# Optimization experiments

Measured on AMD Instinct MI355X. Metric: run time of the kernel, lower is better.

The kernel has to match this reference:

```python
import jax, jax.numpy as jnp
import numpy as np

IN_CH = 64
NODE = 48
K_NEIGS = 10
KERNEL = 5
STRIDE = 2
BN_EPS = 1e-5


def _local_kernel(size, k, s):
    idx = np.arange(size * size).reshape(size, size)
    win = np.lib.stride_tricks.sliding_window_view(idx, (k, k))[::s, ::s]
    patches = win.reshape(-1, k * k)  # [n_edges, k*k] pixel indices
    n_edges = patches.shape[0]
    H = np.zeros((size * size, n_edges), dtype=np.float32)
    H[patches.reshape(-1), np.repeat(np.arange(n_edges), k * k)] = 1.0
    return jnp.asarray(H)


def _pairwise_distance(x):
    # (B,N,C) -> (B,N,N) squared euclidean
    xsq = jnp.sum(x * x, axis=-1, keepdims=True)
    return xsq - 2.0 * jnp.einsum('bnc,bmc->bnm', x, x) + jnp.swapaxes(xsq, 1, 2)


def _batched_knn(x, k):
    d = _pairwise_distance(x)
    avg = d.mean(-1, keepdims=True)
    neg_vals, inds = jax.lax.top_k(-d, k + 1)  # smallest k+1, sorted ascending
    return -neg_vals, inds, d, avg


def _incidence(inds, N):
    # weights_function(prob=False) == ones; scatter ones then transpose
    B, _, K = inds.shape
    b = jnp.arange(B)[:, None, None]
    p = jnp.arange(N)[None, :, None]
    M = jnp.zeros((B, N, N), dtype=jnp.float32).at[b, p, inds].set(1.0)
    return jnp.swapaxes(M, 1, 2)


def _generate_G(H):
    # G = diag(DV^-0.5) @ H @ I @ diag(DE^-1) @ H^T @ diag(DV^-0.5)
    DV = H.sum(axis=2)  # (B,N)
    DE = H.sum(axis=1)  # (B,E)
    dv2 = DV ** -0.5
    Hs = H * (1.0 / DE)[:, None, :]
    M = jnp.einsum('bne,bme->bnm', Hs, H)
    return dv2[:, :, None] * M * dv2[:, None, :]


def _build_G(x, local_H):
    B, N, C = x.shape
    _, topk_inds, _, _ = _batched_knn(x, K_NEIGS)
    H1 = _incidence(topk_inds, N)
    Dv = H1.sum(axis=2, keepdims=True)  # alpha = 1.0
    max_k = int(jnp.max(Dv))  # data-dependent width (eager, matches torch)
    _, ti2, _, _ = _batched_knn(x, max_k - 1)  # (B,N,max_k)
    tk = jnp.arange(max_k)[None, None, :]
    rng = jnp.broadcast_to(jnp.arange(N)[None, :, None], (B, N, max_k))
    new_inds = jnp.where(tk >= Dv, rng, ti2)
    new_H = _incidence(new_inds, N)
    loc = jnp.broadcast_to(local_H[None], (B,) + local_H.shape)
    return _generate_G(jnp.concatenate([new_H, loc], axis=2))


def _hgnn(x, G, W, b, gamma, beta):
    h = jnp.einsum('bnc,oc->bno', x, W) + b  # Linear
    h = jnp.einsum('bnm,bmc->bnc', G, h)
    mean = h.mean(axis=(0, 1))  # BatchNorm1d over (B,N) per channel
    var = h.var(axis=(0, 1))
    h = gamma * (h - mean) / jnp.sqrt(var + BN_EPS) + beta
    return jax.nn.relu(h) + x


def setup_inputs() -> dict:
    key = jax.random.key(0)
    k1, k2, k3 = jax.random.split(key, 3)
    B, N, C = 4, NODE * NODE, IN_CH
    x = jax.random.normal(k1, (B, N, C), dtype=jnp.float32)
    W = jax.random.normal(k2, (C, C), dtype=jnp.float32) / np.sqrt(C)
    b = jax.random.normal(k3, (C,), dtype=jnp.float32) * 0.01
    gamma = jnp.ones((C,), dtype=jnp.float32)
    beta = jnp.zeros((C,), dtype=jnp.float32)
    return {"x": x, "W": W, "b": b, "gamma": gamma, "beta": beta}


def reference(x, W, b, gamma, beta):
    local_H = _local_kernel(NODE, KERNEL, STRIDE)
    G = _build_G(x, local_H)  # graph construction is no_grad in torch
    return _hgnn(x, G, W, b, gamma, beta)
```

## Files before the change

### kernel.cpp

```cpp
#include <hip/hip_runtime.h>


#define HB    4
#define HN    2304
#define HC    64
#define HK    11
#define HL    48
#define HW    22
#define HE2   484
#define HE    (HN + HE2)
#define HRPB  4
#define NSLOT 36
#define NPAIRS (HB * HK * HN)

__global__ void hg14_sentinel(float* out, int n) {
    int i = blockIdx.x * 256 + threadIdx.x;
    if (i < n) out[i] = 12345.0f;
}

__global__ void hg14_init(int* Dv, int* indeg, float* bnsum, float* bnss) {
    int i = blockIdx.x * 256 + threadIdx.x;
    if (i < HB * HN) { Dv[i] = 0; indeg[i] = 0; }
    if (i < HC) { bnsum[i] = 0.f; bnss[i] = 0.f; }
}

__global__ __launch_bounds__(64) void hg14_linear(const float* x, const float* W,
                                                  const float* bias, float* h1,
                                                  float* xsq, float* xT) {
    int row = blockIdx.x;
    int t = threadIdx.x;
    __shared__ float xr[HC];
    float v = x[row * HC + t];
    xr[t] = v;
    __syncthreads();
    float sq = v * v;
    #pragma unroll
    for (int o = 32; o > 0; o >>= 1) sq += __shfl_xor(sq, o);
    if (t == 0) xsq[row] = sq;
    int b = row / HN, n = row % HN;
    xT[(b * HC + t) * HN + n] = v;
    float acc = bias[t];
    #pragma unroll 8
    for (int c = 0; c < HC; c++) acc += xr[c] * W[t * HC + c];
    h1[row * HC + t] = acc;
}

__device__ __forceinline__ unsigned hg14_wave_min_u32(unsigned v) {
    #pragma unroll
    for (int o = 32; o > 0; o >>= 1) {
        unsigned ov = __shfl_xor(v, o);
        v = ov < v ? ov : v;
    }
    return v;
}

#define HG14_INS4(q0, q1, q2, q3, x)                                     \
    {                                                                    \
        unsigned long long x_ = (x), n_;                                 \
        n_ = q0 < x_ ? q0 : x_; x_ = q0 < x_ ? x_ : q0; q0 = n_;         \
        n_ = q1 < x_ ? q1 : x_; x_ = q1 < x_ ? x_ : q1; q1 = n_;         \
        n_ = q2 < x_ ? q2 : x_; x_ = q2 < x_ ? x_ : q2; q2 = n_;         \
        if (x_ < q3) q3 = x_;                                            \
    }

#define HG14_CE(u, v)                                                    \
    { unsigned long long t_ = u < v ? u : v; v = u < v ? v : u; u = t_; }

#define HG14_BUILD()                                                               \
    {                                                                              \
        unsigned long long a0 = CINF, a1 = CINF, a2 = CINF, a3 = CINF;             \
        unsigned long long b0 = CINF, b1 = CINF, b2 = CINF, b3 = CINF;             \
        _Pragma("unroll")                                                          \
        for (int s = 0; s < NSLOT / 2; s++) {                                      \
            unsigned long long pa = ((unsigned long long)key[s] << 12) |           \
                                    (unsigned)((s << 6) | lane);                   \
            unsigned long long pb = ((unsigned long long)key[s + 18] << 12) |      \
                                    (unsigned)(((s + 18) << 6) | lane);            \
            HG14_INS4(a0, a1, a2, a3, pa);                                         \
            HG14_INS4(b0, b1, b2, b3, pb);                                         \
        }                                                                          \
        c0 = a0 < b3 ? a0 : b3; c1 = a1 < b2 ? a1 : b2;                            \
        c2 = a2 < b1 ? a2 : b1; c3 = a3 < b0 ? a3 : b0;                            \
        HG14_CE(c0, c2); HG14_CE(c1, c3); HG14_CE(c0, c1); HG14_CE(c2, c3);        \
    }

#define HG14_EXTRACT(kk, EMIT)                                                     \
    {                                                                              \
        for (int j = 0; j < (kk); j++) {                                           \
            unsigned hk = (unsigned)(c0 >> 12);                                    \
            unsigned mk = hg14_wave_min_u32(hk);                                   \
            unsigned long long bal = __ballot(hk == mk);                           \
            bool iswin;                                                            \
            if (__popcll(bal) == 1) {                                              \
                iswin = (hk == mk);                                                \
            } else {                                                               \
                unsigned mc = (hk == mk) ? (unsigned)(c0 & 0xFFFu) : 0xFFFFFFFFu;  \
                unsigned mm = hg14_wave_min_u32(mc);                               \
                iswin = (mc == mm);                                                \
            }                                                                      \
            if (iswin) {                                                           \
                int bi = (int)(c0 & 0xFFFu);                                       \
                EMIT;                                                              \
                unsigned long long popped = c0;                                    \
                c0 = c1; c1 = c2; c2 = c3; c3 = CINF;                              \
                if (c0 == CINF) {                                                  \
                    _Pragma("unroll")                                              \
                    for (int s = 0; s < NSLOT; s++) {                              \
                        unsigned long long pk =                                    \
                            ((unsigned long long)key[s] << 12) |                   \
                            (unsigned)((s << 6) | lane);                           \
                        if (pk > popped) HG14_INS4(c0, c1, c2, c3, pk);            \
                    }                                                              \
                }                                                                  \
            }                                                                      \
        }                                                                          \
    }

__device__ __forceinline__ void hg14_kth(const unsigned (&key)[NSLOT], int kk,
                                         unsigned& T, int& cntLess, int& take) {
    unsigned andv = 0xFFFFFFFFu, orv = 0u;
    #pragma unroll
    for (int s = 0; s < NSLOT; s++) { andv &= key[s]; orv |= key[s]; }
    #pragma unroll
    for (int o = 32; o > 0; o >>= 1) {
        andv &= (unsigned)__shfl_xor((int)andv, o);
        orv  |= (unsigned)__shfl_xor((int)orv, o);
    }
    unsigned diff = andv ^ orv;
    if (diff == 0u) { T = andv; cntLess = 0; take = kk; return; }
    int tstart = 31 - __builtin_clz(diff);
    unsigned lowmask = (tstart == 31) ? 0xFFFFFFFFu : ((1u << (tstart + 1)) - 1u);
    unsigned pref = andv & ~lowmask;
    int r = kk;
    for (int t = tstart; t >= 0; t--) {
        unsigned pt = pref >> t;
        int c = 0;
        #pragma unroll
        for (int s = 0; s < NSLOT; s++) c += ((key[s] >> t) == pt) ? 1 : 0;
        #pragma unroll
        for (int o = 32; o > 0; o >>= 1) c += __shfl_xor(c, o);
        if (r > c) { r -= c; pref |= (1u << t); }
    }
    T = pref; cntLess = kk - r; take = r;
}

__device__ __forceinline__ void hg14_scan64(int v, int lane, int& excl, int& total) {
    int inc = v;
    #pragma unroll
    for (int o = 1; o < 64; o <<= 1) {
        int u = __shfl_up(inc, o);
        if (lane >= o) inc += u;
    }
    excl = inc - v;
    total = __shfl(inc, 63);
}

#define HG24_R4(qq, ss, ww)                                              \
    qq.x += (ss) * ww.x; qq.y += (ss) * ww.y;                            \
    qq.z += (ss) * ww.z; qq.w += (ss) * ww.w;

#define HG24_ST4(row, qq, sv, mm)                                              \
    *reinterpret_cast<float4*>(&d[row][(mm)]) =                                \
        make_float4(xs[row] + sv.x - 2.f * qq.x, xs[row] + sv.y - 2.f * qq.y,  \
                    xs[row] + sv.z - 2.f * qq.z, xs[row] + sv.w - 2.f * qq.w);

__global__ __launch_bounds__(256) void hg24_knn_count(const float* xT, const float* xsq,
                                                      int* Dv, unsigned int* kcache,
                                                      int storekeys) {
    __shared__ float d[HRPB][HN];
    __shared__ __align__(16) float xrt[HC][HRPB];
    const int t = threadIdx.x;
    const int b = blockIdx.x / (HN / HRPB);
    const int n0 = (blockIdx.x % (HN / HRPB)) * HRPB;
    const int r = t >> 6;
    const int lane = t & 63;
    xrt[lane][r] = xT[(b * HC + lane) * HN + n0 + r];
    __syncthreads();
    float xs[HRPB];
    #pragma unroll
    for (int q = 0; q < HRPB; q++) xs[q] = xsq[b * HN + n0 + q];

    {
        const int m = 4 * t;
        float4 q0a = {0.f,0.f,0.f,0.f}, q0b = {0.f,0.f,0.f,0.f};
        float4 q1a = {0.f,0.f,0.f,0.f}, q1b = {0.f,0.f,0.f,0.f};
        float4 q2a = {0.f,0.f,0.f,0.f}, q2b = {0.f,0.f,0.f,0.f};
        float4 q3a = {0.f,0.f,0.f,0.f}, q3b = {0.f,0.f,0.f,0.f};
        #pragma unroll 8
        for (int c = 0; c < HC; c++) {
            float4 xq = *reinterpret_cast<const float4*>(&xrt[c][0]);
            const float* bp = &xT[(b * HC + c) * HN + m];
            float4 ua = *reinterpret_cast<const float4*>(bp);
            float4 ub = *reinterpret_cast<const float4*>(bp + 1024);
            HG24_R4(q0a, xq.x, ua); HG24_R4(q0b, xq.x, ub);
            HG24_R4(q1a, xq.y, ua); HG24_R4(q1b, xq.y, ub);
            HG24_R4(q2a, xq.z, ua); HG24_R4(q2b, xq.z, ub);
            HG24_R4(q3a, xq.w, ua); HG24_R4(q3b, xq.w, ub);
        }
        float4 s0 = *reinterpret_cast<const float4*>(&xsq[b * HN + m]);
        float4 s1 = *reinterpret_cast<const float4*>(&xsq[b * HN + m + 1024]);
        HG24_ST4(0, q0a, s0, m); HG24_ST4(0, q0b, s1, m + 1024);
        HG24_ST4(1, q1a, s0, m); HG24_ST4(1, q1b, s1, m + 1024);
        HG24_ST4(2, q2a, s0, m); HG24_ST4(2, q2b, s1, m + 1024);
        HG24_ST4(3, q3a, s0, m); HG24_ST4(3, q3b, s1, m + 1024);
    }
    if (t < 64) {
        const int m = 2048 + 4 * t;
        float4 q0 = {0.f,0.f,0.f,0.f}, q1 = {0.f,0.f,0.f,0.f};
        float4 q2 = {0.f,0.f,0.f,0.f}, q3 = {0.f,0.f,0.f,0.f};
        #pragma unroll 8
        for (int c = 0; c < HC; c++) {
            float4 xq = *reinterpret_cast<const float4*>(&xrt[c][0]);
            float4 ua = *reinterpret_cast<const float4*>(&xT[(b * HC + c) * HN + m]);
            HG24_R4(q0, xq.x, ua); HG24_R4(q1, xq.y, ua);
            HG24_R4(q2, xq.z, ua); HG24_R4(q3, xq.w, ua);
        }
        float4 s0 = *reinterpret_cast<const float4*>(&xsq[b * HN + m]);
        HG24_ST4(0, q0, s0, m); HG24_ST4(1, q1, s0, m);
        HG24_ST4(2, q2, s0, m); HG24_ST4(3, q3, s0, m);
    }
    __syncthreads();

    const int p = n0 + r;
    const unsigned long long CINF = ~0ull;
    unsigned int key[NSLOT];
    unsigned long long c0, c1, c2, c3;
    const int rowbase = (b * HN + p) * NSLOT;
    #pragma unroll
    for (int s = 0; s < NSLOT; s++) {
        float f = d[r][(s << 6) | lane];
        unsigned int ub = __float_as_uint(f);
        unsigned int k = ub ^ (((unsigned int)(((int)ub) >> 31)) | 0x80000000u);
        key[s] = k;
        if (storekeys) kcache[(rowbase + s) * 64 + lane] = k;
    }
    HG14_BUILD();
    HG14_EXTRACT(HK, atomicAdd(&Dv[b * HN + bi], 1));
}

__global__ __launch_bounds__(256) void hg15_scan(const int* Dv, int* offs) {
    __shared__ int wsum[4];
    int t = threadIdx.x;
    int lane = t & 63, w = t >> 6;
    int base = t * 36;
    int s = 0;
    for (int i = 0; i < 36; i++) s += max(Dv[base + i], 1);
    int inc = s;
    #pragma unroll
    for (int o = 1; o < 64; o <<= 1) {
        int u = __shfl_up(inc, o);
        if (lane >= o) inc += u;
    }
    if (lane == 63) wsum[w] = inc;
    __syncthreads();
    int woff = 0;
    for (int i = 0; i < w; i++) woff += wsum[i];
    int acc = woff + inc - s;
    for (int i = 0; i < 36; i++) { offs[base + i] = acc; acc += max(Dv[base + i], 1); }
}

__device__ __forceinline__ void hg14_select_emit(const unsigned (&key)[NSLOT],
                                                 int b, int p, int lane, int kk, int base,
                                                 int* indeg, unsigned int* pairs) {
    unsigned T; int cntLess, take;
    hg14_kth(key, kk, T, cntLess, take);
    int cl = 0;
    #pragma unroll
    for (int s = 0; s < NSLOT; s++) cl += (key[s] < T) ? 1 : 0;
    int off, tot;
    hg14_scan64(cl, lane, off, tot);
    int w = 0;
    #pragma unroll
    for (int s = 0; s < NSLOT; s++) {
        if (key[s] < T) {
            int m = (s << 6) | lane;
            atomicAdd(&indeg[b * HN + m], 1);
            pairs[base + off + w] =
                ((unsigned)b << 24) | ((unsigned)p << 12) | (unsigned)m;
            w++;
        }
    }
    int lastm = -1;
    for (int t2 = 0; t2 < take; t2++) {
        int mc = 0x7FFFFFFF;
        #pragma unroll
        for (int s = 0; s < NSLOT; s++) {
            int m = (s << 6) | lane;
            if (key[s] == T && m > lastm && m < mc) mc = m;
        }
        int mmin = mc;
        #pragma unroll
        for (int o = 32; o > 0; o >>= 1) {
            int ov = __shfl_xor(mmin, o);
            mmin = ov < mmin ? ov : mmin;
        }
        if (mc == mmin) {
            atomicAdd(&indeg[b * HN + mmin], 1);
            pairs[base + cntLess + t2] =
                ((unsigned)b << 24) | ((unsigned)p << 12) | (unsigned)mmin;
        }
        lastm = mmin;
    }
}

__global__ __launch_bounds__(256) void hg14_knn_sel_cached(const unsigned int* kcache,
                                                           const int* Dv, const int* offs,
                                                           int* indeg, unsigned int* pairs) {
    const int t = threadIdx.x;
    const int lane = t & 63;
    const int gw = blockIdx.x * HRPB + (t >> 6);
    const int b = gw / HN, p = gw % HN;
    unsigned int key[NSLOT];
    const int rowbase = gw * NSLOT;
    #pragma unroll
    for (int s = 0; s < NSLOT; s++) key[s] = kcache[(rowbase + s) * 64 + lane];
    hg14_select_emit(key, b, p, lane, max(Dv[gw], 1), offs[gw], indeg, pairs);
}

__global__ __launch_bounds__(256) void hg14_knn_sel_full(const float* xT, const float* xsq,
                                                         const int* Dv, const int* offs,
                                                         int* indeg, unsigned int* pairs) {
    __shared__ float d[HRPB][HN];
    __shared__ float xr[HRPB][HC];
    const int t = threadIdx.x;
    const int b = blockIdx.x / (HN / HRPB);
    const int n0 = (blockIdx.x % (HN / HRPB)) * HRPB;
    const int r = t >> 6;
    const int lane = t & 63;
    xr[r][lane] = xT[(b * HC + lane) * HN + n0 + r];
    __syncthreads();
    float xs[HRPB];
    #pragma unroll
    for (int q = 0; q < HRPB; q++) xs[q] = xsq[b * HN + n0 + q];
    for (int m = t; m < HN; m += 256) {
        float dot0 = 0.f, dot1 = 0.f, dot2 = 0.f, dot3 = 0.f;
        #pragma unroll 8
        for (int c = 0; c < HC; c++) {
            float xv = xT[(b * HC + c) * HN + m];
            dot0 += xr[0][c] * xv;
            dot1 += xr[1][c] * xv;
            dot2 += xr[2][c] * xv;
            dot3 += xr[3][c] * xv;
        }
        float xsm = xsq[b * HN + m];
        d[0][m] = xs[0] + xsm - 2.f * dot0;
        d[1][m] = xs[1] + xsm - 2.f * dot1;
        d[2][m] = xs[2] + xsm - 2.f * dot2;
        d[3][m] = xs[3] + xsm - 2.f * dot3;
    }
    __syncthreads();
    const int p = n0 + r;
    unsigned int key[NSLOT];
    #pragma unroll
    for (int s = 0; s < NSLOT; s++) {
        float f = d[r][(s << 6) | lane];
        unsigned int ub = __float_as_uint(f);
        key[s] = ub ^ (((unsigned int)(((int)ub) >> 31)) | 0x80000000u);
    }
    const int gw = b * HN + p;
    hg14_select_emit(key, b, p, lane, max(Dv[gw], 1), offs[gw], indeg, pairs);
}

__device__ __forceinline__ int hg14_lo(int rc) { return max(0, (rc - 3) / 2); }
__device__ __forceinline__ int hg14_hi(int rc) { return min(HW - 1, rc / 2); }

__global__ __launch_bounds__(256) void hg14_scale(float* h1, const int* indeg) {
    int i = blockIdx.x * 256 + threadIdx.x;
    int node = i >> 6;
    int n = node % HN;
    int r = n / HL, c = n % HL;
    int cover = max(0, hg14_hi(r) - hg14_lo(r) + 1) * max(0, hg14_hi(c) - hg14_lo(c) + 1);
    int dvn = max(indeg[node] + cover, 1);
    h1[i] *= rsqrtf((float)dvn);
}

__global__ void hg14_zero(float* z, float* h2) {
    int i = blockIdx.x * 256 + threadIdx.x;
    int b = i / (HN * HC), rem = i % (HN * HC);
    z[b * HE * HC + rem] = 0.f;
    h2[i] = 0.f;
}

__global__ __launch_bounds__(256) void hg14_edge(const unsigned int* pairs, const int* Dv,
                                                 const float* y, float* z) {
    int wv = (blockIdx.x * 256 + threadIdx.x) >> 6;
    int lane = threadIdx.x & 63;
    if (wv < NPAIRS) {
        unsigned int pk = pairs[wv];
        int b = pk >> 24;
        if (b >= HB) return;
        int p = (pk >> 12) & 0xFFF, m = pk & 0xFFF;
        float invde = 1.f / (float)max(Dv[b * HN + p], 1);
        atomicAdd(&z[(b * HE + p) * HC + lane], y[(b * HN + m) * HC + lane] * invde);
    } else {
        int w2 = wv - NPAIRS;
        if (w2 >= HB * HE2) return;
        int b = w2 / HE2, w = w2 % HE2;
        int wr = w / HW, wc = w % HW;
        float acc = 0.f;
        #pragma unroll
        for (int i = 0; i < 5; i++)
            #pragma unroll
            for (int j = 0; j < 5; j++)
                acc += y[(b * HN + (wr * 2 + i) * HL + wc * 2 + j) * HC + lane];
        z[(b * HE + HN + w) * HC + lane] = acc * (1.f / 25.f);
    }
}

__global__ __launch_bounds__(256) void hg14_gscatter(const unsigned int* pairs,
                                                     const float* z, float* h2) {
    int idx = (blockIdx.x * 256 + threadIdx.x) >> 6;
    int lane = threadIdx.x & 63;
    if (idx >= NPAIRS) return;
    unsigned int pk = pairs[idx];
    int b = pk >> 24;
    if (b >= HB) return;
    int p = (pk >> 12) & 0xFFF, m = pk & 0xFFF;
    atomicAdd(&h2[(b * HN + m) * HC + lane], z[(b * HE + p) * HC + lane]);
}

__global__ __launch_bounds__(256) void hg14_gfinish(const float* z, const int* indeg, float* h2) {
    int wave = (blockIdx.x * 256 + threadIdx.x) >> 6;
    int lane = threadIdx.x & 63;
    int b = wave / HN, n = wave % HN;
    int g = b * HN + n;
    float acc = h2[g * HC + lane];
    int r = n / HL, c = n % HL;
    int rlo = hg14_lo(r), rhi = hg14_hi(r), clo = hg14_lo(c), chi = hg14_hi(c);
    for (int wr = rlo; wr <= rhi; wr++)
        for (int wc = clo; wc <= chi; wc++)
            acc += z[(b * HE + HN + wr * HW + wc) * HC + lane];
    int dvn = max(indeg[g] + max(0, rhi - rlo + 1) * max(0, chi - clo + 1), 1);
    h2[g * HC + lane] = acc * rsqrtf((float)dvn);
}

__global__ __launch_bounds__(256) void hg14_bnstats(const float* h2, float* bnsum, float* bnss) {
    int t = threadIdx.x;
    int c = t & 63, rg = t >> 6;
    int row0 = blockIdx.x * 36;
    float s = 0.f, ss = 0.f;
    for (int r = rg; r < 36; r += 4) {
        float v = h2[(row0 + r) * HC + c];
        s += v; ss += v * v;
    }
    __shared__ float ls[256], lss[256];
    ls[t] = s; lss[t] = ss;
    __syncthreads();
    if (t < 64) {
        s  = ls[t]  + ls[t + 64]  + ls[t + 128]  + ls[t + 192];
        ss = lss[t] + lss[t + 64] + lss[t + 128] + lss[t + 192];
        atomicAdd(&bnsum[t], s);
        atomicAdd(&bnss[t], ss);
    }
}

__global__ __launch_bounds__(256) void hg14_final(const float* h2, const float* x,
                                                  const float* gamma, const float* beta,
                                                  const float* bnsum, const float* bnss,
                                                  float* out) {
    int i = blockIdx.x * 256 + threadIdx.x;
    int c = i & 63;
    const float M = (float)(HB * HN);
    float mean = bnsum[c] / M;
    float var  = bnss[c] / M - mean * mean;
    float inv  = rsqrtf(var + 1e-5f);
    float h = gamma[c] * (h2[i] - mean) * inv + beta[c];
    out[i] = fmaxf(h, 0.f) + x[i];
}

extern "C" void kernel_launch(void* const* d_in, const int* in_sizes, int n_in,
                              void* d_out, int out_size, void* d_ws, size_t ws_size,
                              hipStream_t stream) {
    const float* x     = (const float*)d_in[0];
    const float* W     = (const float*)d_in[1];
    const float* bias  = (const float*)d_in[2];
    const float* gamma = (const float*)d_in[3];
    const float* beta  = (const float*)d_in[4];
    float* out = (float*)d_out;
    (void)in_sizes; (void)n_in;

    char* ws = (char*)d_ws;
    size_t off = 0;
    float*        xsq     = (float*)(ws + off);        off += (size_t)HB * HN * 4;
    float*        h1      = (float*)(ws + off);        off += (size_t)HB * HN * HC * 4;
    float*        h2      = (float*)(ws + off);        off += (size_t)HB * HN * HC * 4;
    int*          Dv      = (int*)(ws + off);          off += (size_t)HB * HN * 4;
    int*          indeg   = (int*)(ws + off);          off += (size_t)HB * HN * 4;
    int*          offs    = (int*)(ws + off);          off += (size_t)HB * HN * 4;
    unsigned int* pairs   = (unsigned int*)(ws + off); off += (size_t)NPAIRS * 4;
    float*        bnsum   = (float*)(ws + off);        off += 256;
    float*        bnss    = (float*)(ws + off);        off += 256;
    float*        xT      = (float*)(ws + off);
    float*        z       = (float*)(ws + off);
    off += (size_t)HB * HE * HC * 4;
    size_t base_need = off;
    unsigned int* kcache  = (unsigned int*)(ws + off);
    size_t cache_need = off + (size_t)HB * HN * NSLOT * 64 * 4;

    if (ws_size < base_need) {
        hg14_sentinel<<<(out_size + 255) / 256, 256, 0, stream>>>(out, out_size);
        return;
    }
    const int use_cache = (ws_size >= cache_need) ? 1 : 0;

    const int EDGE_WAVES = NPAIRS + HB * HE2;

    hg14_init<<<(HB * HN + 255) / 256, 256, 0, stream>>>(Dv, indeg, bnsum, bnss);
    hg14_linear<<<HB * HN, 64, 0, stream>>>(x, W, bias, h1, xsq, xT);
    hg24_knn_count<<<HB * (HN / HRPB), 256, 0, stream>>>(xT, xsq, Dv, kcache, use_cache);
    hg15_scan<<<1, 256, 0, stream>>>(Dv, offs);
    if (use_cache)
        hg14_knn_sel_cached<<<HB * (HN / HRPB), 256, 0, stream>>>(kcache, Dv, offs, indeg, pairs);
    else
        hg14_knn_sel_full<<<HB * (HN / HRPB), 256, 0, stream>>>(xT, xsq, Dv, offs, indeg, pairs);
    hg14_scale<<<(HB * HN * HC) / 256, 256, 0, stream>>>(h1, indeg);
    hg14_zero<<<(HB * HN * HC) / 256, 256, 0, stream>>>(z, h2);
    hg14_edge<<<EDGE_WAVES / 4, 256, 0, stream>>>(pairs, Dv, h1, z);
    hg14_gscatter<<<(NPAIRS * 64) / 256, 256, 0, stream>>>(pairs, z, h2);
    hg14_gfinish<<<(HB * HN) / 4, 256, 0, stream>>>(z, indeg, h2);
    hg14_bnstats<<<256, 256, 0, stream>>>(h2, bnsum, bnss);
    hg14_final<<<(HB * HN * HC) / 256, 256, 0, stream>>>(h2, x, gamma, beta, bnsum, bnss, out);
}
```

Baseline: 348.6 us.

## Fuse init, scan, scale and zero kernels into neighbouring kernels

New measurement: 408.5 us. 1.17x slower.

```diff
diff --git a/kernel.cpp b/kernel.cpp
--- a/kernel.cpp
+++ b/kernel.cpp
@@ -18,17 +18,18 @@
     if (i < n) out[i] = 12345.0f;
 }
 
-__global__ void hg14_init(int* Dv, int* indeg, float* bnsum, float* bnss) {
-    int i = blockIdx.x * 256 + threadIdx.x;
-    if (i < HB * HN) { Dv[i] = 0; indeg[i] = 0; }
-    if (i < HC) { bnsum[i] = 0.f; bnss[i] = 0.f; }
-}
-
-__global__ __launch_bounds__(64) void hg14_linear(const float* x, const float* W,
+__global__ __launch_bounds__(64) void hg25_linear(const float* x, const float* W,
                                                   const float* bias, float* h1,
-                                                  float* xsq, float* xT) {
+                                                  float* xsq, float* xT,
+                                                  int* Dv, int* indeg, int* cursor,
+                                                  float* bnsum, float* bnss) {
     int row = blockIdx.x;
     int t = threadIdx.x;
+    if (t == 0) { Dv[row] = 0; indeg[row] = 0; }
+    if (row == 0) {
+        bnsum[t] = 0.f; bnss[t] = 0.f;
+        if (t == 0) *cursor = 0;
+    }
     __shared__ float xr[HC];
     float v = x[row * HC + t];
     xr[t] = v;
@@ -238,27 +239,6 @@
     HG14_EXTRACT(HK, atomicAdd(&Dv[b * HN + bi], 1));
 }
 
-__global__ __launch_bounds__(256) void hg15_scan(const int* Dv, int* offs) {
-    __shared__ int wsum[4];
-    int t = threadIdx.x;
-    int lane = t & 63, w = t >> 6;
-    int base = t * 36;
-    int s = 0;
-    for (int i = 0; i < 36; i++) s += max(Dv[base + i], 1);
-    int inc = s;
-    #pragma unroll
-    for (int o = 1; o < 64; o <<= 1) {
-        int u = __shfl_up(inc, o);
-        if (lane >= o) inc += u;
-    }
-    if (lane == 63) wsum[w] = inc;
-    __syncthreads();
-    int woff = 0;
-    for (int i = 0; i < w; i++) woff += wsum[i];
-    int acc = woff + inc - s;
-    for (int i = 0; i < 36; i++) { offs[base + i] = acc; acc += max(Dv[base + i], 1); }
-}
-
 __device__ __forceinline__ void hg14_select_emit(const unsigned (&key)[NSLOT],
                                                  int b, int p, int lane, int kk, int base,
                                                  int* indeg, unsigned int* pairs) {
@@ -303,23 +283,30 @@
     }
 }
 
-__global__ __launch_bounds__(256) void hg14_knn_sel_cached(const unsigned int* kcache,
-                                                           const int* Dv, const int* offs,
-                                                           int* indeg, unsigned int* pairs) {
+__global__ __launch_bounds__(256) void hg25_sel(const unsigned int* kcache,
+                                                const int* Dv, int* cursor,
+                                                int* indeg, unsigned int* pairs,
+                                                float* z, float* h2) {
     const int t = threadIdx.x;
     const int lane = t & 63;
     const int gw = blockIdx.x * HRPB + (t >> 6);
     const int b = gw / HN, p = gw % HN;
+    h2[gw * HC + lane] = 0.f;
+    z[(b * HE + p) * HC + lane] = 0.f;
     unsigned int key[NSLOT];
     const int rowbase = gw * NSLOT;
     #pragma unroll
     for (int s = 0; s < NSLOT; s++) key[s] = kcache[(rowbase + s) * 64 + lane];
-    hg14_select_emit(key, b, p, lane, max(Dv[gw], 1), offs[gw], indeg, pairs);
-}
-
-__global__ __launch_bounds__(256) void hg14_knn_sel_full(const float* xT, const float* xsq,
-                                                         const int* Dv, const int* offs,
-                                                         int* indeg, unsigned int* pairs) {
+    int kk = max(Dv[gw], 1);
+    int base = 0;
+    if (lane == 0) base = atomicAdd(cursor, kk);
+    base = __shfl(base, 0);
+    hg14_select_emit(key, b, p, lane, kk, base, indeg, pairs);
+}
+
+__global__ __launch_bounds__(256) void hg25_sel_full(const float* xT, const float* xsq,
+                                                     const int* Dv, int* cursor,
+                                                     int* indeg, unsigned int* pairs) {
     __shared__ float d[HRPB][HN];
     __shared__ float xr[HRPB][HC];
     const int t = threadIdx.x;
@@ -358,20 +345,11 @@
         key[s] = ub ^ (((unsigned int)(((int)ub) >> 31)) | 0x80000000u);
     }
     const int gw = b * HN + p;
-    hg14_select_emit(key, b, p, lane, max(Dv[gw], 1), offs[gw], indeg, pairs);
-}
-
-__device__ __forceinline__ int hg14_lo(int rc) { return max(0, (rc - 3) / 2); }
-__device__ __forceinline__ int hg14_hi(int rc) { return min(HW - 1, rc / 2); }
-
-__global__ __launch_bounds__(256) void hg14_scale(float* h1, const int* indeg) {
-    int i = blockIdx.x * 256 + threadIdx.x;
-    int node = i >> 6;
-    int n = node % HN;
-    int r = n / HL, c = n % HL;
-    int cover = max(0, hg14_hi(r) - hg14_lo(r) + 1) * max(0, hg14_hi(c) - hg14_lo(c) + 1);
-    int dvn = max(indeg[node] + cover, 1);
-    h1[i] *= rsqrtf((float)dvn);
+    int kk = max(Dv[gw], 1);
+    int base = 0;
+    if (lane == 0) base = atomicAdd(cursor, kk);
+    base = __shfl(base, 0);
+    hg14_select_emit(key, b, p, lane, kk, base, indeg, pairs);
 }
 
 __global__ void hg14_zero(float* z, float* h2) {
@@ -381,8 +359,18 @@
     h2[i] = 0.f;
 }
 
-__global__ __launch_bounds__(256) void hg14_edge(const unsigned int* pairs, const int* Dv,
-                                                 const float* y, float* z) {
+__device__ __forceinline__ int hg14_lo(int rc) { return max(0, (rc - 3) / 2); }
+__device__ __forceinline__ int hg14_hi(int rc) { return min(HW - 1, rc / 2); }
+
+__device__ __forceinline__ float hg25_s(const int* indeg, int b, int n) {
+    int r = n / HL, c = n % HL;
+    int cover = max(0, hg14_hi(r) - hg14_lo(r) + 1) * max(0, hg14_hi(c) - hg14_lo(c) + 1);
+    int dvn = max(indeg[b * HN + n] + cover, 1);
+    return rsqrtf((float)dvn);
+}
+
+__global__ __launch_bounds__(256) void hg25_edge(const unsigned int* pairs, const int* Dv,
+                                                 const int* indeg, const float* y, float* z) {
     int wv = (blockIdx.x * 256 + threadIdx.x) >> 6;
     int lane = threadIdx.x & 63;
     if (wv < NPAIRS) {
@@ -391,7 +379,9 @@
         if (b >= HB) return;
         int p = (pk >> 12) & 0xFFF, m = pk & 0xFFF;
         float invde = 1.f / (float)max(Dv[b * HN + p], 1);
-        atomicAdd(&z[(b * HE + p) * HC + lane], y[(b * HN + m) * HC + lane] * invde);
+        float sc = hg25_s(indeg, b, m);
+        atomicAdd(&z[(b * HE + p) * HC + lane],
+                  (y[(b * HN + m) * HC + lane] * sc) * invde);
     } else {
         int w2 = wv - NPAIRS;
         if (w2 >= HB * HE2) return;
@@ -401,8 +391,10 @@
         #pragma unroll
         for (int i = 0; i < 5; i++)
             #pragma unroll
-            for (int j = 0; j < 5; j++)
-                acc += y[(b * HN + (wr * 2 + i) * HL + wc * 2 + j) * HC + lane];
+            for (int j = 0; j < 5; j++) {
+                int n2 = (wr * 2 + i) * HL + wc * 2 + j;
+                acc += y[(b * HN + n2) * HC + lane] * hg25_s(indeg, b, n2);
+            }
         z[(b * HE + HN + w) * HC + lane] = acc * (1.f / 25.f);
     }
 }
@@ -486,7 +478,7 @@
     float*        h2      = (float*)(ws + off);        off += (size_t)HB * HN * HC * 4;
     int*          Dv      = (int*)(ws + off);          off += (size_t)HB * HN * 4;
     int*          indeg   = (int*)(ws + off);          off += (size_t)HB * HN * 4;
-    int*          offs    = (int*)(ws + off);          off += (size_t)HB * HN * 4;
+    int*          cursor  = (int*)(ws + off);          off += 256;
     unsigned int* pairs   = (unsigned int*)(ws + off); off += (size_t)NPAIRS * 4;
     float*        bnsum   = (float*)(ws + off);        off += 256;
     float*        bnss    = (float*)(ws + off);        off += 256;
@@ -505,17 +497,18 @@
 
     const int EDGE_WAVES = NPAIRS + HB * HE2;
 
-    hg14_init<<<(HB * HN + 255) / 256, 256, 0, stream>>>(Dv, indeg, bnsum, bnss);
-    hg14_linear<<<HB * HN, 64, 0, stream>>>(x, W, bias, h1, xsq, xT);
+    hg25_linear<<<HB * HN, 64, 0, stream>>>(x, W, bias, h1, xsq, xT,
+                                            Dv, indeg, cursor, bnsum, bnss);
     hg24_knn_count<<<HB * (HN / HRPB), 256, 0, stream>>>(xT, xsq, Dv, kcache, use_cache);
-    hg15_scan<<<1, 256, 0, stream>>>(Dv, offs);
-    if (use_cache)
-        hg14_knn_sel_cached<<<HB * (HN / HRPB), 256, 0, stream>>>(kcache, Dv, offs, indeg, pairs);
-    else
-        hg14_knn_sel_full<<<HB * (HN / HRPB), 256, 0, stream>>>(xT, xsq, Dv, offs, indeg, pairs);
-    hg14_scale<<<(HB * HN * HC) / 256, 256, 0, stream>>>(h1, indeg);
-    hg14_zero<<<(HB * HN * HC) / 256, 256, 0, stream>>>(z, h2);
-    hg14_edge<<<EDGE_WAVES / 4, 256, 0, stream>>>(pairs, Dv, h1, z);
+    if (use_cache) {
+        hg25_sel<<<HB * (HN / HRPB), 256, 0, stream>>>(kcache, Dv, cursor, indeg,
+                                                       pairs, z, h2);
+    } else {
+        hg25_sel_full<<<HB * (HN / HRPB), 256, 0, stream>>>(xT, xsq, Dv, cursor,
+                                                            indeg, pairs);
+        hg14_zero<<<(HB * HN * HC) / 256, 256, 0, stream>>>(z, h2);
+    }
+    hg25_edge<<<EDGE_WAVES / 4, 256, 0, stream>>>(pairs, Dv, indeg, h1, z);
     hg14_gscatter<<<(NPAIRS * 64) / 256, 256, 0, stream>>>(pairs, z, h2);
     hg14_gfinish<<<(HB * HN) / 4, 256, 0, stream>>>(z, indeg, h2);
     hg14_bnstats<<<256, 256, 0, stream>>>(h2, bnsum, bnss);
```
